# Kernel tuning notes

Measured on AMD Instinct MI355X. Metric: run time of the kernel, lower is better.

The kernel has to match this reference:

```python
import jax, jax.numpy as jnp
import numpy as np

CHEB_K = 2; HORIZON = 12; HFS = 4; D_HEAD = 32; EPS = 1e-5

def layer_norm(x, g, b):
    mu = x.mean(-1, keepdims=True)
    v = ((x - mu) ** 2).mean(-1, keepdims=True)
    return (x - mu) * jax.lax.rsqrt(v + EPS) * g + b

def gconv(x, supports, W, b):
    # x:[B,N,C], supports:[K,N,N], W:[N,K,C,O], b:[N,O]
    xg = jnp.einsum('knm,bmc->bnkc', supports, x)
    return jnp.einsum('bnkc,nkco->bno', xg, W) + b

def run_layer(x, state0, supports, gW, gb, uW, ub):
    # x:[B,T,N,C] -> hidden states [B,T,N,H] via GRU-style adaptive graph-conv recurrence
    def step(state, xt):
        xs = jnp.concatenate([xt, state], -1)
        zr = jax.nn.sigmoid(gconv(xs, supports, gW, gb))
        z, r = jnp.split(zr, 2, -1)
        hc = jnp.tanh(gconv(jnp.concatenate([xt, z * state], -1), supports, uW, ub))
        h = r * state + (1.0 - r) * hc
        return h, h
    _, hs = jax.lax.scan(step, state0, x.transpose(1, 0, 2, 3))
    return hs.transpose(1, 0, 2, 3)

def setup_inputs():
    key = jax.random.key(0)
    B, T, N, Din, H, E = 32, 12, 512, 2, 64, 16
    ks = iter(jax.random.split(key, 40))
    def rn(shape, scale):
        return jax.random.normal(next(ks), shape, jnp.float32) * scale
    inp = {}
    inp['source'] = rn((B, T, N, Din), 1.0)
    inp['targets'] = rn((B, T, N, 1), 1.0)
    inp['node_emb'] = rn((N, E), 1.0)
    for l, din in enumerate([Din, H]):
        c = din + H
        inp['gate_wpool_%d' % l] = rn((E, CHEB_K, c, 2 * H), (E * CHEB_K * c) ** -0.5)
        inp['gate_bpool_%d' % l] = rn((E, 2 * H), E ** -0.5)
        inp['upd_wpool_%d' % l] = rn((E, CHEB_K, c, H), (E * CHEB_K * c) ** -0.5)
        inp['upd_bpool_%d' % l] = rn((E, H), E ** -0.5)
    hyp_in = CHEB_K * H * CHEB_K * H
    inp['hyp_W'] = rn((hyp_in, HORIZON * HFS), hyp_in ** -0.5)
    inp['hyp_b'] = rn((HORIZON * HFS,), 0.02)
    for nm in ['Wq', 'Wk', 'Wv', 'ffW1', 'ffW2']:
        inp[nm] = rn((H, H), H ** -0.5)
    for nm in ['bq', 'bk', 'bv', 'ffb1', 'ffb2']:
        inp[nm] = jnp.zeros((H,), jnp.float32)
    inp['ln1_g'] = jnp.ones((H,), jnp.float32); inp['ln1_b'] = jnp.zeros((H,), jnp.float32)
    inp['ln2_g'] = jnp.ones((H,), jnp.float32); inp['ln2_b'] = jnp.zeros((H,), jnp.float32)
    inp['fc_W'] = rn((H, 1), H ** -0.5)
    inp['fc_b'] = jnp.zeros((1,), jnp.float32)
    return inp

def reference(source, targets, node_emb, gate_wpool_0, gate_bpool_0, upd_wpool_0, upd_bpool_0,
              gate_wpool_1, gate_bpool_1, upd_wpool_1, upd_bpool_1, hyp_W, hyp_b,
              Wq, bq, Wk, bk, Wv, bv, ln1_g, ln1_b, ffW1, ffb1, ffW2, ffb2, ln2_g, ln2_b, fc_W, fc_b):
    B, T, N, _ = source.shape
    H = Wq.shape[0]
    # adaptive supports (cheb_k = 2): [I, softmax(relu(E @ E^T), dim=1)]
    adj = jax.nn.softmax(jax.nn.relu(node_emb @ node_emb.T), axis=1)
    supports = jnp.stack([jnp.eye(N, dtype=source.dtype), adj], 0)  # [K,N,N]
    state0 = jnp.zeros((B, N, H), source.dtype)
    out = source
    for (gwp, gbp, uwp, ubp) in [(gate_wpool_0, gate_bpool_0, upd_wpool_0, upd_bpool_0),
                                 (gate_wpool_1, gate_bpool_1, upd_wpool_1, upd_bpool_1)]:
        gW = jnp.einsum('ne,ekio->nkio', node_emb, gwp); gb = node_emb @ gbp
        uW = jnp.einsum('ne,ekio->nkio', node_emb, uwp); ub = node_emb @ ubp
        out = run_layer(out, state0, supports, gW, gb, uW, ub)
        last_uW = uW  # encoder returns last layer's candidate-gconv per-node weights
    # Hypernetwork: dilation=0 grouped 1xHFS conv == scale last hidden state by sum of filter taps
    hlin = last_uW.reshape(N, -1) @ hyp_W + hyp_b               # [N, horizon*HFS]
    fs = hlin.reshape(N, HORIZON, HFS).sum(-1)                  # [N, horizon]
    h = jnp.einsum('bnh,nt->btnh', out[:, -1], fs)              # [B, horizon, N, H]
    # Transform attention block (L = 1; loop re-uses same `out`, only last iter matters)
    heads = H // D_HEAD
    q = out @ Wq + bq; k = out @ Wk + bk; v = h @ Wv + bv
    def split_heads(t):
        return t.reshape(B, T, N, heads, D_HEAD).transpose(3, 0, 2, 1, 4)  # [h,B,N,T,d]
    q, k, v = split_heads(q), split_heads(k), split_heads(v)
    A = jax.nn.softmax(jnp.einsum('hbntd,hbnsd->hbnts', q, k) / (D_HEAD ** 0.5), axis=-1)
    o = jnp.einsum('hbnts,hbnsd->hbntd', A, v)
    o = o.transpose(1, 3, 2, 0, 4).reshape(B, T, N, H)
    val = layer_norm(o + out, ln1_g, ln1_b)
    ffo = jnp.maximum(val @ ffW1 + ffb1, 0.0) @ ffW2 + ffb2
    out_h = layer_norm(ffo + val, ln2_g, ln2_b)
    y = (out_h @ fc_W + fc_b)[..., 0]                           # [B,T,N]
    y = y.reshape(-1, HORIZON, 1, N).transpose(0, 1, 3, 2)      # [B,horizon,N,1]
    return y
```

## Files before the change

### kernel.cpp

```cpp
#include <hip/hip_runtime.h>
#include <hip/hip_bf16.h>


using bf16 = __hip_bfloat16;
#define B2F(x) __bfloat162float(x)

#define NN 512
#define BBATCH 32
#define HHID 64
#define TT 12
#define EE 16

typedef __attribute__((ext_vector_type(4))) float f32x4;
typedef __attribute__((ext_vector_type(8))) short bf16x8;

__device__ inline float wsum(float x) {
#pragma unroll
  for (int off = 32; off > 0; off >>= 1) x += __shfl_xor(x, off, 64);
  return x;
}

__device__ inline uint4 llc_load4(const void* p) {
  uint4 r;
  asm volatile("global_load_dwordx4 %0, %1, off sc0 sc1" : "=v"(r) : "v"(p));
  return r;
}
__device__ inline uint2 llc_load2(const void* p) {
  uint2 r;
  asm volatile("global_load_dwordx2 %0, %1, off sc0 sc1" : "=v"(r) : "v"(p));
  return r;
}
__device__ inline unsigned llc_load1(const void* p) {
  unsigned r;
  asm volatile("global_load_dword %0, %1, off sc0 sc1" : "=v"(r) : "v"(p));
  return r;
}
__device__ inline void llc_store_bf(void* p, unsigned short v) {
  asm volatile("global_store_short %0, %1, off sc0 sc1" :: "v"(p), "v"((unsigned)v) : "memory");
}
__device__ inline void llc_store_u1(void* p, unsigned v) {
  asm volatile("global_store_dword %0, %1, off sc0 sc1" :: "v"(p), "v"(v) : "memory");
}
template <int N> __device__ inline void wait_vmcnt() {
  if constexpr (N == 0) asm volatile("s_waitcnt vmcnt(0)" ::: "memory");
  else if constexpr (N == 1) asm volatile("s_waitcnt vmcnt(1)" ::: "memory");
  else if constexpr (N == 2) asm volatile("s_waitcnt vmcnt(2)" ::: "memory");
  else asm volatile("s_waitcnt vmcnt(4)" ::: "memory");
}

__device__ inline void lds_barrier() {
  asm volatile("s_waitcnt lgkmcnt(0)" ::: "memory");
  __builtin_amdgcn_s_barrier();
  asm volatile("" ::: "memory");
}

__device__ inline void gbar(unsigned* __restrict__ bar, int& cnt) {
  cnt++;
  __syncthreads();
  unsigned tgt = (unsigned)cnt;
  unsigned* flags = bar + 32;
  if (blockIdx.x == 0) {
    if (threadIdx.x < 64) {
      if (threadIdx.x == 0) llc_store_u1(flags, tgt);
      const unsigned* fp = flags + threadIdx.x * 8;
      bool ok;
      do {
        unsigned v0 = llc_load1(fp + 0), v1 = llc_load1(fp + 1),
                 v2 = llc_load1(fp + 2), v3 = llc_load1(fp + 3),
                 v4 = llc_load1(fp + 4), v5 = llc_load1(fp + 5),
                 v6 = llc_load1(fp + 6), v7 = llc_load1(fp + 7);
        wait_vmcnt<0>();
        __builtin_amdgcn_sched_barrier(0);
        ok = ((int)(v0 - tgt) >= 0) && ((int)(v1 - tgt) >= 0) &&
             ((int)(v2 - tgt) >= 0) && ((int)(v3 - tgt) >= 0) &&
             ((int)(v4 - tgt) >= 0) && ((int)(v5 - tgt) >= 0) &&
             ((int)(v6 - tgt) >= 0) && ((int)(v7 - tgt) >= 0);
      } while (!__all(ok));
      if (threadIdx.x == 0) llc_store_u1(bar, tgt);
    }
  } else if (threadIdx.x == 0) {
    llc_store_u1(flags + blockIdx.x, tgt);
    for (;;) {
      unsigned e = llc_load1(bar);
      wait_vmcnt<0>();
      __builtin_amdgcn_sched_barrier(0);
      if ((int)(e - tgt) >= 0) break;
      __builtin_amdgcn_s_sleep(2);
    }
  }
  __syncthreads();
}

__global__ __launch_bounds__(256) void zero_f32_kernel(float* __restrict__ p, int n) {
  int i = blockIdx.x * 256 + threadIdx.x;
  if (i < n) p[i] = 0.0f;
}


__global__ __launch_bounds__(256) void adj_kernel(const float* __restrict__ emb,
                                                  bf16* __restrict__ adjb) {
  __shared__ float embAll[NN * EE];
  __shared__ float red[256];
  int tid = threadIdx.x, n = blockIdx.x;
  for (int i = tid; i < NN * EE; i += 256) embAll[i] = emb[i];
  __syncthreads();
  float v[2];
#pragma unroll
  for (int j = 0; j < 2; j++) {
    int m = tid + j * 256;
    float s = 0.f;
#pragma unroll
    for (int e = 0; e < EE; e++) s += embAll[n * EE + e] * embAll[m * EE + e];
    v[j] = fmaxf(s, 0.0f);
  }
  float mx = fmaxf(v[0], v[1]);
  red[tid] = mx; __syncthreads();
  for (int s = 128; s > 0; s >>= 1) { if (tid < s) red[tid] = fmaxf(red[tid], red[tid + s]); __syncthreads(); }
  mx = red[0]; __syncthreads();
  float e0 = expf(v[0] - mx), e1 = expf(v[1] - mx);
  red[tid] = e0 + e1; __syncthreads();
  for (int s = 128; s > 0; s >>= 1) { if (tid < s) red[tid] += red[tid + s]; __syncthreads(); }
  float inv = 1.0f / red[0];
  adjb[n * NN + tid] = __float2bfloat16(e0 * inv);
  adjb[n * NN + tid + 256] = __float2bfloat16(e1 * inv);
}

__global__ __launch_bounds__(256) void wgen_kernel(const float* __restrict__ pool,
                                                   const float* __restrict__ emb,
                                                   float* __restrict__ out, int J) {
  __shared__ float embL[128 * EE];
  int tid = threadIdx.x;
  int n0 = blockIdx.y * 128;
  for (int i = tid; i < 128 * EE; i += 256) embL[i] = emb[n0 * EE + i];
  __syncthreads();
  int j = blockIdx.x * 256 + tid;
  if (j >= J) return;
  float pw[EE];
#pragma unroll
  for (int e = 0; e < EE; e++) pw[e] = pool[e * J + j];
#pragma unroll 4
  for (int nn = 0; nn < 128; nn++) {
    float s = 0.f;
#pragma unroll
    for (int e = 0; e < EE; e++) s += embL[nn * EE + e] * pw[e];
    out[(size_t)(n0 + nn) * J + j] = s;
  }
}

__global__ __launch_bounds__(256) void wgen_t_kernel(const float* __restrict__ pool,
                                                     const float* __restrict__ emb,
                                                     bf16* __restrict__ out, int J,
                                                     int O, int KCP, int KC) {
  __shared__ float embL[128 * EE];
  int tid = threadIdx.x;
  int n0 = blockIdx.y * 128;
  for (int i = tid; i < 128 * EE; i += 256) embL[i] = emb[n0 * EE + i];
  __syncthreads();
  int p = blockIdx.x * 256 + tid;
  unsigned kc = (unsigned)p % (unsigned)KCP;
  unsigned o = (unsigned)p / (unsigned)KCP;
  size_t P = (size_t)KCP * O;
  if (kc >= (unsigned)KC) {
    bf16 z = __float2bfloat16(0.f);
    for (int nn = 0; nn < 128; nn++) out[(size_t)(n0 + nn) * P + p] = z;
    return;
  }
  int jp = (int)kc * O + (int)o;
  float pw[EE];
#pragma unroll
  for (int e = 0; e < EE; e++) pw[e] = pool[e * J + jp];
#pragma unroll 4
  for (int nn = 0; nn < 128; nn++) {
    float s = 0.f;
#pragma unroll
    for (int e = 0; e < EE; e++) s += embL[nn * EE + e] * pw[e];
    out[(size_t)(n0 + nn) * P + p] = __float2bfloat16(s);
  }
}

__global__ __launch_bounds__(256) void pw_kernel(const float* __restrict__ upool,
                                                 const float* __restrict__ hypW,
                                                 float* __restrict__ PW) {
  __shared__ float red[256];
  int j = blockIdx.x, e = blockIdx.y, tid = threadIdx.x;
  float s = 0.f;
#pragma unroll 4
  for (int p = tid; p < 16384; p += 256) s += upool[e * 16384 + p] * hypW[p * 48 + j];
  red[tid] = s; __syncthreads();
  for (int t = 128; t > 0; t >>= 1) { if (tid < t) red[tid] += red[tid + t]; __syncthreads(); }
  if (tid == 0) PW[e * 48 + j] = red[0];
}

__global__ __launch_bounds__(256) void fs_kernel(const float* __restrict__ emb,
                                                 const float* __restrict__ PW,
                                                 const float* __restrict__ hypb,
                                                 float* __restrict__ fs) {
  int id = blockIdx.x * 256 + threadIdx.x;
  if (id >= NN * TT) return;
  int n = id / TT, t = id % TT;
  float s = 0.f;
#pragma unroll
  for (int f = 0; f < 4; f++) {
    int j = t * 4 + f;
    float h = hypb[j];
#pragma unroll
    for (int e = 0; e < EE; e++) h += emb[n * EE + e] * PW[e * 48 + j];
    s += h;
  }
  fs[id] = s;
}

__global__ __launch_bounds__(256) void cvt_src_kernel(const float* __restrict__ src,
                                                      bf16* __restrict__ x) {
  int id = blockIdx.x * 256 + threadIdx.x;
  int c = id & 1, b = (id >> 1) & 31, n = (id >> 6) & 511, t = id >> 15;
  x[id] = __float2bfloat16(src[((b * TT + t) * NN + n) * 2 + c]);
}

#define DBUF 4672

__device__ inline void xsT_wr8(unsigned short* xsT, int base, int q0l, int k, uint4 v) {
  union { uint4 u; unsigned short h[8]; } cv; cv.u = v;
#pragma unroll
  for (int qq = 0; qq < 8; qq++) {
    int q = q0l + qq;
    xsT[base + q * 72 + (q >> 3) * 8 + k] = cv.h[qq];
  }
}

template <int QW>
__device__ inline void diffuse_tileP(const bf16x8* __restrict__ apre,
                                     const bf16* __restrict__ X, bf16* __restrict__ Y,
                                     int Q, int n0, int q0, char* smraw, int tid) {
  constexpr int LPC = QW / 32;
  constexpr int NCT = QW / 16;
  unsigned short* xsT = (unsigned short*)smraw;
  int w = tid >> 6, lane = tid & 63;
  int col = lane & 15, quad = lane >> 4;
  int kr, ql;
  if constexpr (QW == 64) { kr = tid >> 3; ql = (tid & 7) * 8; }
  else                    { kr = tid >> 2; ql = (tid & 3) * 8; }
  f32x4 acc[NCT];
#pragma unroll
  for (int ct = 0; ct < NCT; ct++) acc[ct] = (f32x4){0.f, 0.f, 0.f, 0.f};
  const bf16* Xb = X + q0 + ql;
  uint4 pre[3][LPC];
#pragma unroll
  for (int d = 0; d < 3; d++) {
    pre[d][0] = llc_load4(Xb + (size_t)(d * 64 + kr) * Q);
    if constexpr (QW == 64)
      pre[d][1] = llc_load4(Xb + (size_t)(d * 64 + 32 + kr) * Q);
  }
  wait_vmcnt<2 * LPC>();
  xsT_wr8(xsT, 0, ql, kr, pre[0][0]);
  if constexpr (QW == 64) xsT_wr8(xsT, 0, ql, 32 + kr, pre[0][1]);
  pre[0][0] = llc_load4(Xb + (size_t)(3 * 64 + kr) * Q);
  if constexpr (QW == 64)
    pre[0][1] = llc_load4(Xb + (size_t)(3 * 64 + 32 + kr) * Q);
  lds_barrier();
#pragma unroll
  for (int c = 0; c < 8; c++) {
    int sl = (c + 1) % 3;
    if (c < 7) {
      if (c < 5) wait_vmcnt<2 * LPC>();
      else if (c == 5) wait_vmcnt<LPC>();
      else wait_vmcnt<0>();
      int nb = ((c + 1) & 1) * DBUF;
      xsT_wr8(xsT, nb, ql, kr, pre[sl][0]);
      if constexpr (QW == 64) xsT_wr8(xsT, nb, ql, 32 + kr, pre[sl][1]);
    }
    int base = (c & 1) * DBUF;
#pragma unroll
    for (int ki = 0; ki < 2; ki++) {
      bf16x8 a = apre[c * 2 + ki];
#pragma unroll
      for (int ct = 0; ct < NCT; ct++) {
        int q = ct * 16 + col;
        bf16x8 b = *(const bf16x8*)&xsT[base + q * 72 + (q >> 3) * 8 + ki * 32 + quad * 8];
        acc[ct] = __builtin_amdgcn_mfma_f32_16x16x32_bf16(a, b, acc[ct], 0, 0, 0);
      }
    }
    if (c + 4 < 8) {
      pre[sl][0] = llc_load4(Xb + (size_t)((c + 4) * 64 + kr) * Q);
      if constexpr (QW == 64)
        pre[sl][1] = llc_load4(Xb + (size_t)((c + 4) * 64 + 32 + kr) * Q);
    }
    lds_barrier();
  }
#pragma unroll
  for (int ct = 0; ct < NCT; ct++)
#pragma unroll
    for (int r = 0; r < 4; r++) {
      int row = n0 + w * 16 + quad * 4 + r;
      bf16 hb = __float2bfloat16(acc[ct][r]);
      llc_store_bf(Y + (size_t)row * Q + q0 + ct * 16 + col, *(unsigned short*)&hb);
    }
}


template <int C>
__device__ inline void stage_A(int n, int tid, unsigned short* xinb,
    const bf16* __restrict__ xt, const bf16* __restrict__ xd,
    const bf16* __restrict__ sa, const bf16* __restrict__ sad) {
  constexpr int cc = C + HHID, KC = 2 * cc, KCP = (KC + 31) & ~31, PIT = KCP + 8;
  __syncthreads();
  for (int i = tid; i < 32 * KCP; i += 256) {
    int b = i / KCP, kc = i - b * KCP;
    unsigned short v = 0;
    if (kc < C)            v = *(const unsigned short*)&xt[(n * 32 + b) * C + kc];
    else if (kc < cc)      v = *(const unsigned short*)&sa[(n * 32 + b) * HHID + kc - C];
    else if (kc < cc + C)  v = *(const unsigned short*)&xd[(n * 32 + b) * C + kc - cc];
    else if (kc < KC)      v = *(const unsigned short*)&sad[(n * 32 + b) * HHID + kc - cc - C];
    xinb[b * PIT + kc] = v;
  }
  __syncthreads();
}

template <int C>
__device__ inline void gate_epilogue(int n, int w, int col, int quad,
    f32x4 acc[2][2], const float* __restrict__ gb, const float* __restrict__ state,
    bf16* __restrict__ zs, bf16* __restrict__ rbuf) {
#pragma unroll
  for (int i = 0; i < 2; i++) {
    int o = (w + i * 4) * 16 + col;
    float bv = gb[n * 128 + o];
#pragma unroll
    for (int mt = 0; mt < 2; mt++)
#pragma unroll
      for (int r = 0; r < 4; r++) {
        int m = mt * 16 + quad * 4 + r;
        float zr = 1.0f / (1.0f + expf(-(acc[i][mt][r] + bv)));
        int idx = (n * 32 + m) * HHID + (o & 63);
        if (o < HHID) zs[idx] = __float2bfloat16(zr * state[idx]);
        else          rbuf[idx] = __float2bfloat16(zr);
      }
  }
}

template <int C>
__device__ inline void upd_epilogue(int n, int w, int col, int quad,
    f32x4 acc[2], const float* __restrict__ ub, float* __restrict__ state,
    bf16* __restrict__ sb, const bf16* __restrict__ rbuf, bf16* __restrict__ xo) {
  int o = w * 16 + col;
  float bv = ub[n * 64 + o];
#pragma unroll
  for (int mt = 0; mt < 2; mt++)
#pragma unroll
    for (int r = 0; r < 4; r++) {
      int m = mt * 16 + quad * 4 + r;
      int idx = (n * 32 + m) * HHID + o;
      float hc = tanhf(acc[mt][r] + bv);
      float rr = B2F(rbuf[idx]);
      float st = state[idx];
      float h = rr * st + (1.0f - rr) * hc;
      state[idx] = h;
      bf16 hb = __float2bfloat16(h);
      sb[idx] = hb;
      xo[idx] = hb;
    }
}

template <int C>
__device__ inline void gate_mfma(int n, int tid, const unsigned short* xinb,
    const bf16* __restrict__ gWt, const float* __restrict__ gb,
    const float* __restrict__ state, bf16* __restrict__ zs, bf16* __restrict__ rbuf) {
  constexpr int KC = 2 * (C + HHID), KCP = (KC + 31) & ~31, PIT = KCP + 8;
  int w = tid >> 6, lane = tid & 63, col = lane & 15, quad = lane >> 4;
  f32x4 acc[2][2];
#pragma unroll
  for (int i = 0; i < 2; i++)
#pragma unroll
    for (int mt = 0; mt < 2; mt++) acc[i][mt] = (f32x4){0.f, 0.f, 0.f, 0.f};
  const bf16* Wn = gWt + (size_t)n * KCP * 128;
#pragma unroll 2
  for (int k0 = 0; k0 < KCP; k0 += 32) {
    int ko = k0 + quad * 8;
    bf16x8 a0 = *(const bf16x8*)&xinb[col * PIT + ko];
    bf16x8 a1 = *(const bf16x8*)&xinb[(16 + col) * PIT + ko];
#pragma unroll
    for (int i = 0; i < 2; i++) {
      int o = (w + i * 4) * 16 + col;
      bf16x8 bf = *(const bf16x8*)(Wn + (size_t)o * KCP + ko);
      acc[i][0] = __builtin_amdgcn_mfma_f32_16x16x32_bf16(a0, bf, acc[i][0], 0, 0, 0);
      acc[i][1] = __builtin_amdgcn_mfma_f32_16x16x32_bf16(a1, bf, acc[i][1], 0, 0, 0);
    }
  }
  gate_epilogue<C>(n, w, col, quad, acc, gb, state, zs, rbuf);
}

template <int C>
__device__ inline void upd_mfma(int n, int tid, const unsigned short* xinb,
    const bf16* __restrict__ uWt, const float* __restrict__ ub,
    float* __restrict__ state, bf16* __restrict__ sb,
    const bf16* __restrict__ rbuf, bf16* __restrict__ xo) {
  constexpr int KC = 2 * (C + HHID), KCP = (KC + 31) & ~31, PIT = KCP + 8;
  int w = tid >> 6, lane = tid & 63, col = lane & 15, quad = lane >> 4;
  f32x4 acc[2];
  acc[0] = (f32x4){0.f, 0.f, 0.f, 0.f};
  acc[1] = (f32x4){0.f, 0.f, 0.f, 0.f};
  const bf16* Wn = uWt + (size_t)n * KCP * 64;
  int o = w * 16 + col;
#pragma unroll 2
  for (int k0 = 0; k0 < KCP; k0 += 32) {
    int ko = k0 + quad * 8;
    bf16x8 a0 = *(const bf16x8*)&xinb[col * PIT + ko];
    bf16x8 a1 = *(const bf16x8*)&xinb[(16 + col) * PIT + ko];
    bf16x8 bf = *(const bf16x8*)(Wn + (size_t)o * KCP + ko);
    acc[0] = __builtin_amdgcn_mfma_f32_16x16x32_bf16(a0, bf, acc[0], 0, 0, 0);
    acc[1] = __builtin_amdgcn_mfma_f32_16x16x32_bf16(a1, bf, acc[1], 0, 0, 0);
  }
  upd_epilogue<C>(n, w, col, quad, acc, ub, state, sb, rbuf, xo);
}


template <int C>
__global__ __launch_bounds__(256, 2) void recur_kernel(
    const bf16* __restrict__ adjb, const bf16* __restrict__ xin,
    const bf16* __restrict__ gWt, const float* __restrict__ gb,
    const bf16* __restrict__ uWt, const float* __restrict__ ub,
    bf16* __restrict__ zs, bf16* __restrict__ sdiff, bf16* __restrict__ zsdiff,
    bf16* __restrict__ xd, bf16* __restrict__ xout, unsigned* __restrict__ bar) {
  constexpr int KC = 2 * (C + HHID), KCP = (KC + 31) & ~31, PIT = KCP + 8;
  constexpr int NK = KCP / 32;
  constexpr int QX = 32 * C;
  __shared__ __align__(16) char dsm[2 * DBUF * 2];
  __shared__ __align__(16) unsigned short xinb[32 * PIT];
  int bid = blockIdx.x, tid = threadIdx.x;
  int w = tid >> 6, lane = tid & 63, col = lane & 15, quad = lane >> 4;
  int bcnt = 0;

  bf16x8 apre[16];
  {
    int n0p = ((bid & 255) >> 5) * 64;
    const bf16* ar = adjb + (size_t)(n0p + w * 16 + col) * NN;
#pragma unroll
    for (int c = 0; c < 8; c++)
#pragma unroll
      for (int ki = 0; ki < 2; ki++)
        apre[c * 2 + ki] = *(const bf16x8*)(ar + c * 64 + ki * 32 + quad * 8);
  }
  bf16x8 fg[2 * NK];
  {
    const bf16* Wn = gWt + (size_t)bid * KCP * 128;
#pragma unroll
    for (int i = 0; i < 2; i++) {
      int o = (w + i * 4) * 16 + col;
#pragma unroll
      for (int kk = 0; kk < NK; kk++)
        fg[i * NK + kk] = *(const bf16x8*)(Wn + (size_t)o * KCP + kk * 32 + quad * 8);
    }
  }
  bf16x8 fu[NK];
  {
    const bf16* Wn = uWt + (size_t)bid * KCP * 64;
    int o = w * 16 + col;
#pragma unroll
    for (int kk = 0; kk < NK; kk++)
      fu[kk] = *(const bf16x8*)(Wn + (size_t)o * KCP + kk * 32 + quad * 8);
  }
  float gbv0 = gb[bid * 128 + w * 16 + col];
  float gbv1 = gb[bid * 128 + 64 + w * 16 + col];
  float ubv  = ub[bid * 64 + w * 16 + col];

  for (int i = tid; i < 32 * PIT; i += 256) xinb[i] = 0;
  __syncthreads();

  int r2 = tid >> 3, ch = tid & 7;
  uint4 vxt; unsigned sxt = 0, sxd = 0;
  if constexpr (C == 64) {
    vxt = *(const uint4*)(xin + (size_t)(bid * 32 + r2) * 64 + ch * 8);
  } else {
    if (tid < 32) sxt = *(const unsigned*)(xin + (size_t)(bid * 32 + tid) * 2);
  }

  float st[2][4], rr_[2][4];
#pragma unroll
  for (int mt = 0; mt < 2; mt++)
#pragma unroll
    for (int r4 = 0; r4 < 4; r4++) st[mt][r4] = 0.f;

  if constexpr (C == 2) {
    int wg = (bid & 31) | ((bid >> 8) << 5);
    if (wg < TT)
      diffuse_tileP<64>(apre, xin + (size_t)wg * NN * QX, xd + (size_t)wg * NN * QX,
                        QX, ((bid & 255) >> 5) * 64, 0, dsm, tid);
  } else {
    if (bid >= 256)
      diffuse_tileP<64>(apre, xin, xd, 2048, ((bid & 255) >> 5) * 64,
                        (bid & 31) * 64, dsm, tid);
  }
  gbar(bar, bcnt);

  for (int t = 0; t < TT; t++) {
    const bf16* xt = xin + (size_t)t * NN * QX;
    const bf16* xdt = (C == 2) ? (xd + (size_t)t * NN * QX) : xd;
    bf16* xo = xout + (size_t)t * NN * 32 * HHID;
    if (t > 0) {
      const bf16* sbp = xout + (size_t)(t - 1) * NN * 32 * HHID;
      if constexpr (C == 64) {
        if (bid < 256)
          diffuse_tileP<64>(apre, sbp, sdiff, 2048, (bid >> 5) * 64,
                            (bid & 31) * 64, dsm, tid);
        else
          diffuse_tileP<64>(apre, xt, xd, 2048, ((bid & 255) >> 5) * 64,
                            (bid & 31) * 64, dsm, tid);
      } else {
        int cs = (bid & 31) | ((bid >> 8) << 5);
        diffuse_tileP<32>(apre, sbp, sdiff, 2048, ((bid & 255) >> 5) * 64,
                          cs * 32, dsm, tid);
      }
      gbar(bar, bcnt);
    }
    if constexpr (C == 64) {
      *(uint4*)&xinb[r2 * PIT + ch * 8] = vxt;
      uint4 v1 = llc_load4(xdt + (size_t)(bid * 32 + r2) * 64 + ch * 8);
      uint4 v2;
      if (t > 0) v2 = llc_load4(sdiff + (size_t)(bid * 32 + r2) * 64 + ch * 8);
      wait_vmcnt<0>();
      *(uint4*)&xinb[r2 * PIT + 128 + ch * 8] = v1;
      if (t > 0) *(uint4*)&xinb[r2 * PIT + 192 + ch * 8] = v2;
    } else {
      if (tid < 32) *(unsigned*)&xinb[tid * PIT] = sxt;
      if (t == 0) {
        if (tid < 32) {
          unsigned v = llc_load1(xdt + (size_t)(bid * 32 + tid) * 2);
          wait_vmcnt<0>();
          *(unsigned*)&xinb[tid * PIT + 66] = v;
        }
      } else {
        if (tid >= 32 && tid < 64) *(unsigned*)&xinb[(tid - 32) * PIT + 66] = sxd;
        int r2a = tid >> 4, c4 = tid & 15;
        uint2 va = llc_load2(sdiff + (size_t)(bid * 32 + r2a) * 64 + c4 * 4);
        uint2 vb = llc_load2(sdiff + (size_t)(bid * 32 + 16 + r2a) * 64 + c4 * 4);
        wait_vmcnt<0>();
        *(uint2*)&xinb[r2a * PIT + 68 + c4 * 4] = va;
        *(uint2*)&xinb[(16 + r2a) * PIT + 68 + c4 * 4] = vb;
      }
    }
    __syncthreads();
    {
      f32x4 acc[2][2];
#pragma unroll
      for (int i = 0; i < 2; i++)
#pragma unroll
        for (int mt = 0; mt < 2; mt++) acc[i][mt] = (f32x4){0.f, 0.f, 0.f, 0.f};
#pragma unroll
      for (int kk = 0; kk < NK; kk++) {
        int ko = kk * 32 + quad * 8;
        bf16x8 a0 = *(const bf16x8*)&xinb[col * PIT + ko];
        bf16x8 a1 = *(const bf16x8*)&xinb[(16 + col) * PIT + ko];
#pragma unroll
        for (int i = 0; i < 2; i++) {
          acc[i][0] = __builtin_amdgcn_mfma_f32_16x16x32_bf16(a0, fg[i * NK + kk], acc[i][0], 0, 0, 0);
          acc[i][1] = __builtin_amdgcn_mfma_f32_16x16x32_bf16(a1, fg[i * NK + kk], acc[i][1], 0, 0, 0);
        }
      }
      __syncthreads();
#pragma unroll
      for (int mt = 0; mt < 2; mt++)
#pragma unroll
        for (int r4 = 0; r4 < 4; r4++) {
          int m = mt * 16 + quad * 4 + r4;
          float z = 1.0f / (1.0f + expf(-(acc[0][mt][r4] + gbv0)));
          float rv = 1.0f / (1.0f + expf(-(acc[1][mt][r4] + gbv1)));
          rr_[mt][r4] = rv;
          bf16 zb = __float2bfloat16(z * st[mt][r4]);
          xinb[m * PIT + C + w * 16 + col] = *(unsigned short*)&zb;
          llc_store_bf(zs + (size_t)(bid * 32 + m) * 64 + w * 16 + col,
                       *(unsigned short*)&zb);
        }
    }
    if (t > 0) {
      gbar(bar, bcnt);
      {
        int cs = (bid & 31) | ((bid >> 8) << 5);
        diffuse_tileP<32>(apre, zs, zsdiff, 2048, ((bid & 255) >> 5) * 64,
                          cs * 32, dsm, tid);
      }
      gbar(bar, bcnt);
      if constexpr (C == 64) {
        uint4 v = llc_load4(zsdiff + (size_t)(bid * 32 + r2) * 64 + ch * 8);
        wait_vmcnt<0>();
        *(uint4*)&xinb[r2 * PIT + 192 + ch * 8] = v;
      } else {
        int r2a = tid >> 4, c4 = tid & 15;
        uint2 va = llc_load2(zsdiff + (size_t)(bid * 32 + r2a) * 64 + c4 * 4);
        uint2 vb = llc_load2(zsdiff + (size_t)(bid * 32 + 16 + r2a) * 64 + c4 * 4);
        wait_vmcnt<0>();
        *(uint2*)&xinb[r2a * PIT + 68 + c4 * 4] = va;
        *(uint2*)&xinb[(16 + r2a) * PIT + 68 + c4 * 4] = vb;
      }
    }
    __syncthreads();
    {
      f32x4 acc[2];
      acc[0] = (f32x4){0.f, 0.f, 0.f, 0.f};
      acc[1] = (f32x4){0.f, 0.f, 0.f, 0.f};
#pragma unroll
      for (int kk = 0; kk < NK; kk++) {
        int ko = kk * 32 + quad * 8;
        bf16x8 a0 = *(const bf16x8*)&xinb[col * PIT + ko];
        bf16x8 a1 = *(const bf16x8*)&xinb[(16 + col) * PIT + ko];
        acc[0] = __builtin_amdgcn_mfma_f32_16x16x32_bf16(a0, fu[kk], acc[0], 0, 0, 0);
        acc[1] = __builtin_amdgcn_mfma_f32_16x16x32_bf16(a1, fu[kk], acc[1], 0, 0, 0);
      }
      __syncthreads();
      if (t + 1 < TT) {
        if constexpr (C == 64) {
          vxt = *(const uint4*)(xin + (size_t)(t + 1) * NN * QX +
                                (size_t)(bid * 32 + r2) * 64 + ch * 8);
        } else {
          if (tid < 32)
            sxt = *(const unsigned*)(xin + (size_t)(t + 1) * NN * QX +
                                     (size_t)(bid * 32 + tid) * 2);
          else if (tid < 64)
            sxd = *(const unsigned*)(xd + (size_t)(t + 1) * NN * QX +
                                     (size_t)(bid * 32 + (tid - 32)) * 2);
        }
      }
#pragma unroll
      for (int mt = 0; mt < 2; mt++)
#pragma unroll
        for (int r4 = 0; r4 < 4; r4++) {
          int m = mt * 16 + quad * 4 + r4;
          float hc = tanhf(acc[mt][r4] + ubv);
          float rv = rr_[mt][r4];
          float h = rv * st[mt][r4] + (1.0f - rv) * hc;
          st[mt][r4] = h;
          bf16 hb = __float2bfloat16(h);
          xinb[m * PIT + C + w * 16 + col] = *(unsigned short*)&hb;
          llc_store_bf(xo + (size_t)(bid * 32 + m) * 64 + w * 16 + col,
                       *(unsigned short*)&hb);
        }
    }
    gbar(bar, bcnt);
  }
}


__global__ __launch_bounds__(256, 2) void diffuse0_kernel(const bf16* __restrict__ adjb,
                                                          const bf16* __restrict__ X,
                                                          bf16* __restrict__ Y) {
  __shared__ __align__(16) char smraw[2 * DBUF * 2];
  int bid = blockIdx.x, tid = threadIdx.x;
  int t = bid >> 3, n0 = (bid & 7) * 64;
  int w = tid >> 6, lane = tid & 63, col = lane & 15, quad = lane >> 4;
  bf16x8 ap[16];
  const bf16* ar = adjb + (size_t)(n0 + w * 16 + col) * NN;
#pragma unroll
  for (int c = 0; c < 8; c++)
#pragma unroll
    for (int ki = 0; ki < 2; ki++)
      ap[c * 2 + ki] = *(const bf16x8*)(ar + c * 64 + ki * 32 + quad * 8);
  diffuse_tileP<64>(ap, X + (size_t)t * NN * 64, Y + (size_t)t * NN * 64,
                    64, n0, 0, smraw, tid);
}

__global__ __launch_bounds__(256, 2) void diffuse1_kernel(const bf16* __restrict__ adjb,
                                                          const bf16* __restrict__ X,
                                                          bf16* __restrict__ Y) {
  __shared__ __align__(16) char smraw[2 * DBUF * 2];
  int bid = blockIdx.x, tid = threadIdx.x;
  int n0 = (bid >> 5) * 64;
  int w = tid >> 6, lane = tid & 63, col = lane & 15, quad = lane >> 4;
  bf16x8 ap[16];
  const bf16* ar = adjb + (size_t)(n0 + w * 16 + col) * NN;
#pragma unroll
  for (int c = 0; c < 8; c++)
#pragma unroll
    for (int ki = 0; ki < 2; ki++)
      ap[c * 2 + ki] = *(const bf16x8*)(ar + c * 64 + ki * 32 + quad * 8);
  diffuse_tileP<64>(ap, X, Y, 2048, n0, (bid & 31) * 64, smraw, tid);
}

template <int C>
__global__ __launch_bounds__(256, 2) void gate_wrap(
    const bf16* xt, const bf16* xdt, const bf16* sa, const bf16* sad,
    const bf16* gWt, const float* gb, const float* state, bf16* zs, bf16* rbuf) {
  constexpr int KC = 2 * (C + HHID), KCP = (KC + 31) & ~31, PIT = KCP + 8;
  __shared__ __align__(16) unsigned short xinb[32 * PIT];
  stage_A<C>(blockIdx.x, threadIdx.x, xinb, xt, xdt, sa, sad);
  gate_mfma<C>(blockIdx.x, threadIdx.x, xinb, gWt, gb, state, zs, rbuf);
}

template <int C>
__global__ __launch_bounds__(256, 2) void upd_wrap(
    const bf16* xt, const bf16* xdt, const bf16* sa, const bf16* sad,
    const bf16* uWt, const float* ub, float* state, bf16* sb,
    const bf16* rbuf, bf16* xo) {
  constexpr int KC = 2 * (C + HHID), KCP = (KC + 31) & ~31, PIT = KCP + 8;
  __shared__ __align__(16) unsigned short xinb[32 * PIT];
  stage_A<C>(blockIdx.x, threadIdx.x, xinb, xt, xdt, sa, sad);
  upd_mfma<C>(blockIdx.x, threadIdx.x, xinb, uWt, ub, state, sb, rbuf, xo);
}


#define TP 68

__global__ __launch_bounds__(256, 4) void attn1_kernel(
    const bf16* __restrict__ x1, const float* __restrict__ fsb,
    const float* __restrict__ Wq, const float* __restrict__ bq,
    const float* __restrict__ Wk, const float* __restrict__ bk,
    const float* __restrict__ Wv, const float* __restrict__ bv,
    const float* __restrict__ ln1g, const float* __restrict__ ln1b,
    bf16* __restrict__ val) {
  __shared__ bf16 WqT[4096], WkT[4096];
  __shared__ bf16 Wv_s[4096];
  __shared__ bf16 Xb[16 * 72];
  __shared__ float qs[TT * TP], ks[TT * TP];
  __shared__ float A[2 * TT * TT];
  __shared__ float ovv[64], fss[TT];
  __shared__ float bqs[64], bks[64], bvs[64], g1s[64], b1s[64];
  int tid = threadIdx.x;
  int w = tid >> 6, lane = tid & 63, col = lane & 15, quad = lane >> 4;
#pragma unroll
  for (int i = 0; i < 16; i++) {
    int e = tid * 16 + i;
    int hi = e >> 6, ho = e & 63;
    WqT[ho * 64 + hi] = __float2bfloat16(Wq[e]);
    WkT[ho * 64 + hi] = __float2bfloat16(Wk[e]);
  }
  for (int i = tid; i < 4096; i += 256) Wv_s[i] = __float2bfloat16(Wv[i]);
  for (int i = tid; i < 16 * 72; i += 256) Xb[i] = __float2bfloat16(0.f);
  if (tid < 64) {
    bqs[tid] = bq[tid]; bks[tid] = bk[tid]; bvs[tid] = bv[tid];
    g1s[tid] = ln1g[tid]; b1s[tid] = ln1b[tid];
  }
  __syncthreads();
  for (int g = 0; g < 8; g++) {
    int p = blockIdx.x * 8 + g;
    int b = p >> 9, n = p & 511;
    for (int i = tid; i < TT * 64; i += 256) {
      int t = i >> 6, j = i & 63;
      Xb[t * 72 + j] = x1[(((size_t)t * NN + n) * BBATCH + b) * HHID + j];
    }
    if (tid < TT) fss[tid] = fsb[n * TT + tid];
    __syncthreads();
    {
      f32x4 aq = (f32x4){0.f, 0.f, 0.f, 0.f};
      f32x4 ak = (f32x4){0.f, 0.f, 0.f, 0.f};
#pragma unroll
      for (int ki = 0; ki < 2; ki++) {
        bf16x8 af = *(const bf16x8*)&Xb[col * 72 + ki * 32 + quad * 8];
        bf16x8 bqf = *(const bf16x8*)&WqT[(w * 16 + col) * 64 + ki * 32 + quad * 8];
        bf16x8 bkf = *(const bf16x8*)&WkT[(w * 16 + col) * 64 + ki * 32 + quad * 8];
        aq = __builtin_amdgcn_mfma_f32_16x16x32_bf16(af, bqf, aq, 0, 0, 0);
        ak = __builtin_amdgcn_mfma_f32_16x16x32_bf16(af, bkf, ak, 0, 0, 0);
      }
#pragma unroll
      for (int r = 0; r < 4; r++) {
        int t = quad * 4 + r;
        if (t < TT) {
          int h = w * 16 + col;
          qs[t * TP + h] = aq[r] + bqs[h];
          ks[t * TP + h] = ak[r] + bks[h];
        }
      }
    }
    if (tid < 64) {
      float s = 0.f;
#pragma unroll 8
      for (int j = 0; j < 64; j++)
        s += B2F(Xb[11 * 72 + j]) * B2F(Wv_s[j * 64 + tid]);
      ovv[tid] = s;
    }
    __syncthreads();
    for (int i = tid; i < 2 * TT * TT; i += 256) {
      int hd = i / (TT * TT), ts = i % (TT * TT), t = ts / TT, s = ts % TT;
      float acc = 0.f;
#pragma unroll
      for (int d = 0; d < 32; d++) acc += qs[t * TP + hd * 32 + d] * ks[s * TP + hd * 32 + d];
      A[i] = acc * 0.17677669529663687f;
    }
    __syncthreads();
    if (tid < 2 * TT) {
      int hd = tid / TT, t = tid % TT;
      float* row = &A[hd * TT * TT + t * TT];
      float m = row[0];
      for (int s = 1; s < TT; s++) m = fmaxf(m, row[s]);
      float sm = 0.f;
      for (int s = 0; s < TT; s++) { float e = expf(row[s] - m); row[s] = e; sm += e; }
      float inv = 1.0f / sm;
      for (int s = 0; s < TT; s++) row[s] *= inv;
    }
    __syncthreads();
#pragma unroll
    for (int it = 0; it < 3; it++) {
      int i = it * 256 + tid;
      int t = i >> 6, h = i & 63, hd = h >> 5;
      float afs = 0.f;
#pragma unroll
      for (int s = 0; s < TT; s++) afs += A[hd * TT * TT + t * TT + s] * fss[s];
      float o = ovv[h] * afs + bvs[h];
      float x = o + B2F(Xb[t * 72 + h]);
      float mu = wsum(x) * (1.0f / 64.0f);
      float d = x - mu;
      float var = wsum(d * d) * (1.0f / 64.0f);
      float v = d * rsqrtf(var + 1e-5f) * g1s[h] + b1s[h];
      val[((size_t)(b * TT + t) * NN + n) * HHID + h] = __float2bfloat16(v);
    }
    __syncthreads();
  }
}

__global__ __launch_bounds__(256, 4) void ffn_kernel(
    const bf16* __restrict__ val, const float* __restrict__ W1, const float* __restrict__ b1,
    const float* __restrict__ W2, const float* __restrict__ b2,
    const float* __restrict__ ln2g, const float* __restrict__ ln2b,
    const float* __restrict__ fcW, const float* __restrict__ fcb,
    float* __restrict__ out, int rows_per_block) {
  __shared__ bf16 W1T[4096], W2T[4096];
  __shared__ bf16 Ab[16 * 72];
  __shared__ bf16 Hh[16 * 72], Hl[16 * 72];
  __shared__ float fout[16 * 68];
  __shared__ float b1s[64], b2s[64], g2s[64], bb2[64], fcs[64];
  int tid = threadIdx.x;
  int w = tid >> 6, lane = tid & 63, col = lane & 15, quad = lane >> 4;
#pragma unroll
  for (int i = 0; i < 16; i++) {
    int e = tid * 16 + i;
    int hi = e >> 6, ho = e & 63;
    W1T[ho * 64 + hi] = __float2bfloat16(W1[e]);
    W2T[ho * 64 + hi] = __float2bfloat16(W2[e]);
  }
  if (tid < 64) {
    b1s[tid] = b1[tid]; b2s[tid] = b2[tid];
    g2s[tid] = ln2g[tid]; bb2[tid] = ln2b[tid]; fcs[tid] = fcW[tid];
  }
  __syncthreads();
  float fcbv = fcb[0];
  for (int c0 = 0; c0 < rows_per_block; c0 += 16) {
    size_t r0 = (size_t)blockIdx.x * rows_per_block + c0;
    for (int i = tid; i < 1024; i += 256) {
      int rr = i >> 6, j = i & 63;
      Ab[rr * 72 + j] = val[(r0 + rr) * 64 + j];
    }
    __syncthreads();
    {
      f32x4 a1 = (f32x4){0.f, 0.f, 0.f, 0.f};
#pragma unroll
      for (int ki = 0; ki < 2; ki++) {
        bf16x8 af = *(const bf16x8*)&Ab[col * 72 + ki * 32 + quad * 8];
        bf16x8 bf1 = *(const bf16x8*)&W1T[(w * 16 + col) * 64 + ki * 32 + quad * 8];
        a1 = __builtin_amdgcn_mfma_f32_16x16x32_bf16(af, bf1, a1, 0, 0, 0);
      }
#pragma unroll
      for (int r = 0; r < 4; r++) {
        int m = quad * 4 + r, h = w * 16 + col;
        float hv = fmaxf(a1[r] + b1s[h], 0.0f);
        bf16 hb = __float2bfloat16(hv);
        float lo = hv - B2F(hb);
        Hh[m * 72 + h] = hb;
        Hl[m * 72 + h] = __float2bfloat16(lo);
      }
    }
    __syncthreads();
    {
      f32x4 a2 = (f32x4){0.f, 0.f, 0.f, 0.f};
#pragma unroll
      for (int ki = 0; ki < 2; ki++) {
        bf16x8 ah = *(const bf16x8*)&Hh[col * 72 + ki * 32 + quad * 8];
        bf16x8 al = *(const bf16x8*)&Hl[col * 72 + ki * 32 + quad * 8];
        bf16x8 bf2 = *(const bf16x8*)&W2T[(w * 16 + col) * 64 + ki * 32 + quad * 8];
        a2 = __builtin_amdgcn_mfma_f32_16x16x32_bf16(ah, bf2, a2, 0, 0, 0);
        a2 = __builtin_amdgcn_mfma_f32_16x16x32_bf16(al, bf2, a2, 0, 0, 0);
      }
#pragma unroll
      for (int r = 0; r < 4; r++) {
        int m = quad * 4 + r, h = w * 16 + col;
        fout[m * 68 + h] = a2[r] + b2s[h] + B2F(Ab[m * 72 + h]);
      }
    }
    __syncthreads();
#pragma unroll
    for (int p4 = 0; p4 < 4; p4++) {
      int m = p4 * 4 + w;
      float y = fout[m * 68 + lane];
      float mu = wsum(y) * (1.0f / 64.0f);
      float d = y - mu;
      float var = wsum(d * d) * (1.0f / 64.0f);
      float oh = d * rsqrtf(var + 1e-5f) * g2s[lane] + bb2[lane];
      float contrib = wsum(oh * fcs[lane]);
      if (lane == 0) out[r0 + m] = contrib + fcbv;
    }
    __syncthreads();
  }
}

extern "C" void kernel_launch(void* const* d_in, const int* in_sizes, int n_in,
                              void* d_out, int out_size, void* d_ws, size_t ws_size,
                              hipStream_t stream) {
  const float* src = (const float*)d_in[0];
  const float* emb = (const float*)d_in[2];
  const float* gwp[2] = {(const float*)d_in[3], (const float*)d_in[7]};
  const float* gbp[2] = {(const float*)d_in[4], (const float*)d_in[8]};
  const float* uwp[2] = {(const float*)d_in[5], (const float*)d_in[9]};
  const float* ubp[2] = {(const float*)d_in[6], (const float*)d_in[10]};
  const float* hypW = (const float*)d_in[11];
  const float* hypb = (const float*)d_in[12];
  const float *Wq, *Wk, *Wv, *ffW1, *ffW2, *bq, *bk, *bv, *ffb1, *ffb2;
  const float *ln1g, *ln1b, *ln2g, *ln2b, *fcW, *fcb;
  if (in_sizes[14] == 4096) {
    Wq = (const float*)d_in[13]; Wk = (const float*)d_in[14]; Wv = (const float*)d_in[15];
    ffW1 = (const float*)d_in[16]; ffW2 = (const float*)d_in[17];
    bq = (const float*)d_in[18]; bk = (const float*)d_in[19]; bv = (const float*)d_in[20];
    ffb1 = (const float*)d_in[21]; ffb2 = (const float*)d_in[22];
    ln1g = (const float*)d_in[23]; ln1b = (const float*)d_in[24];
    ln2g = (const float*)d_in[25]; ln2b = (const float*)d_in[26];
    fcW = (const float*)d_in[27]; fcb = (const float*)d_in[28];
  } else {
    Wq = (const float*)d_in[13]; bq = (const float*)d_in[14];
    Wk = (const float*)d_in[15]; bk = (const float*)d_in[16];
    Wv = (const float*)d_in[17]; bv = (const float*)d_in[18];
    ln1g = (const float*)d_in[19]; ln1b = (const float*)d_in[20];
    ffW1 = (const float*)d_in[21]; ffb1 = (const float*)d_in[22];
    ffW2 = (const float*)d_in[23]; ffb2 = (const float*)d_in[24];
    ln2g = (const float*)d_in[25]; ln2b = (const float*)d_in[26];
    fcW = (const float*)d_in[27]; fcb = (const float*)d_in[28];
  }
  float* outp = (float*)d_out;

  char* ws = (char*)d_ws;
  size_t off = 0;
  auto alloc = [&](size_t bytes) {
    void* p = ws + off;
    off += (bytes + 255) & ~(size_t)255;
    return p;
  };
  bf16* adjb = (bf16*)alloc((size_t)512 * 512 * 2);
  bf16* gWb = (bf16*)alloc((size_t)512 * 32768 * 2);
  bf16* uWb = (bf16*)alloc((size_t)512 * 16384 * 2);
  float* gb = (float*)alloc((size_t)512 * 128 * 4);
  float* ub = (float*)alloc((size_t)512 * 64 * 4);
  bf16* xin0 = (bf16*)alloc((size_t)12 * 512 * 32 * 2 * 2);
  bf16* x0 = (bf16*)alloc((size_t)12 * 512 * 32 * 64 * 2);
  bf16* xd0 = (bf16*)alloc((size_t)12 * 512 * 32 * 2 * 2);
  bf16* xdL1 = (bf16*)alloc((size_t)512 * 32 * 64 * 2);
  float* state = (float*)alloc((size_t)512 * 32 * 64 * 4);
  bf16* sb = (bf16*)alloc((size_t)512 * 32 * 64 * 2);
  bf16* sdiff = (bf16*)alloc((size_t)512 * 32 * 64 * 2);
  bf16* zs = (bf16*)alloc((size_t)512 * 32 * 64 * 2);
  bf16* zsdiff = (bf16*)alloc((size_t)512 * 32 * 64 * 2);
  bf16* rbuf = (bf16*)alloc((size_t)512 * 32 * 64 * 2);
  float* PW = (float*)alloc((size_t)16 * 48 * 4);
  float* fsb = (float*)alloc((size_t)512 * 12 * 4);
  unsigned* bar = (unsigned*)alloc((size_t)544 * 4);
  bf16* val = gWb;

  adj_kernel<<<512, 256, 0, stream>>>(emb, adjb);
  pw_kernel<<<dim3(48, 16), 256, 0, stream>>>(uwp[1], hypW, PW);
  fs_kernel<<<24, 256, 0, stream>>>(emb, PW, hypb, fsb);
  cvt_src_kernel<<<1536, 256, 0, stream>>>(src, xin0);

  int occ0 = 0, occ1 = 0;
  hipOccupancyMaxActiveBlocksPerMultiprocessor(&occ0, recur_kernel<2>, 256, 0);
  hipOccupancyMaxActiveBlocksPerMultiprocessor(&occ1, recur_kernel<64>, 256, 0);

  for (int l = 0; l < 2; l++) {
    int C = (l == 0) ? 2 : 64;
    int KC = 2 * (C + 64);
    int KCP = (KC + 31) & ~31;
    int JG = KC * 128, JU = KC * 64;
    wgen_t_kernel<<<dim3(KCP * 128 / 256, 4), 256, 0, stream>>>(
        gwp[l], emb, gWb, JG, 128, KCP, KC);
    wgen_t_kernel<<<dim3(KCP * 64 / 256, 4), 256, 0, stream>>>(
        uwp[l], emb, uWb, JU, 64, KCP, KC);
    wgen_kernel<<<dim3(1, 4), 256, 0, stream>>>(gbp[l], emb, gb, 128);
    wgen_kernel<<<dim3(1, 4), 256, 0, stream>>>(ubp[l], emb, ub, 64);
    zero_f32_kernel<<<3, 256, 0, stream>>>((float*)bar, 544);

    const bf16* xin = (l == 0) ? xin0 : x0;
    bf16* xd = (l == 0) ? xd0 : xdL1;
    int occ = (l == 0) ? occ0 : occ1;
    if (occ >= 2) {
      if (l == 0)
        recur_kernel<2><<<512, 256, 0, stream>>>(adjb, xin, gWb, gb, uWb, ub,
                                                 zs, sdiff, zsdiff, xd, x0, bar);
      else
        recur_kernel<64><<<512, 256, 0, stream>>>(adjb, xin, gWb, gb, uWb, ub,
                                                  zs, sdiff, zsdiff, xd, x0, bar);
    } else {
      zero_f32_kernel<<<4096, 256, 0, stream>>>(state, 512 * 32 * 64);
      zero_f32_kernel<<<2048, 256, 0, stream>>>((float*)sb, 512 * 32 * 64 / 2);
      if (l == 0) diffuse0_kernel<<<96, 256, 0, stream>>>(adjb, xin, xd);
      for (int t = 0; t < 12; t++) {
        const bf16* xt = xin + (size_t)t * 512 * 32 * C;
        const bf16* xdt = (l == 0) ? (xd + (size_t)t * 512 * 32 * C) : xd;
        bf16* xo = x0 + (size_t)t * 512 * 32 * 64;
        if (l == 1) diffuse1_kernel<<<256, 256, 0, stream>>>(adjb, xt, xd);
        diffuse1_kernel<<<256, 256, 0, stream>>>(adjb, sb, sdiff);
        if (l == 0)
          gate_wrap<2><<<512, 256, 0, stream>>>(xt, xdt, sb, sdiff, gWb, gb, state, zs, rbuf);
        else
          gate_wrap<64><<<512, 256, 0, stream>>>(xt, xdt, sb, sdiff, gWb, gb, state, zs, rbuf);
        diffuse1_kernel<<<256, 256, 0, stream>>>(adjb, zs, zsdiff);
        if (l == 0)
          upd_wrap<2><<<512, 256, 0, stream>>>(xt, xdt, zs, zsdiff, uWb, ub, state, sb, rbuf, xo);
        else
          upd_wrap<64><<<512, 256, 0, stream>>>(xt, xdt, zs, zsdiff, uWb, ub, state, sb, rbuf, xo);
      }
    }
  }

  attn1_kernel<<<2048, 256, 0, stream>>>(x0, fsb, Wq, bq, Wk, bk, Wv, bv, ln1g, ln1b, val);
  ffn_kernel<<<2048, 256, 0, stream>>>(val, ffW1, ffb1, ffW2, ffb2, ln2g, ln2b, fcW, fcb,
                                       outp, 96);
}
```

Baseline: 1.651 ms.

## Prefetch all diffusion chunks up front, transpose hypW, and pad weight LDS tiles

The diffusion tile now issues all eight chunk loads at once into an 8-slot register buffer and drains them with decreasing vmcnt waits, replacing the rolling 3-slot prefetch. This gives more memory-level parallelism inside the latency-bound recurrent step, at the cost of extra registers. A new transpose kernel makes the hypW reads in pw_kernel coalesced. The transposed weight tiles in the attention and FFN kernels are padded to a 72-element row stride to cut LDS bank conflicts.

```diff
diff --git a/kernel.cpp b/kernel.cpp
--- a/kernel.cpp
+++ b/kernel.cpp
@@ -42,10 +42,18 @@
   asm volatile("global_store_dword %0, %1, off sc0 sc1" :: "v"(p), "v"(v) : "memory");
 }
 template <int N> __device__ inline void wait_vmcnt() {
-  if constexpr (N == 0) asm volatile("s_waitcnt vmcnt(0)" ::: "memory");
+  if constexpr (N <= 0)      asm volatile("s_waitcnt vmcnt(0)" ::: "memory");
   else if constexpr (N == 1) asm volatile("s_waitcnt vmcnt(1)" ::: "memory");
   else if constexpr (N == 2) asm volatile("s_waitcnt vmcnt(2)" ::: "memory");
-  else asm volatile("s_waitcnt vmcnt(4)" ::: "memory");
+  else if constexpr (N == 3) asm volatile("s_waitcnt vmcnt(3)" ::: "memory");
+  else if constexpr (N == 4) asm volatile("s_waitcnt vmcnt(4)" ::: "memory");
+  else if constexpr (N == 5) asm volatile("s_waitcnt vmcnt(5)" ::: "memory");
+  else if constexpr (N == 6) asm volatile("s_waitcnt vmcnt(6)" ::: "memory");
+  else if constexpr (N == 7) asm volatile("s_waitcnt vmcnt(7)" ::: "memory");
+  else if constexpr (N == 8) asm volatile("s_waitcnt vmcnt(8)" ::: "memory");
+  else if constexpr (N == 10) asm volatile("s_waitcnt vmcnt(10)" ::: "memory");
+  else if constexpr (N == 12) asm volatile("s_waitcnt vmcnt(12)" ::: "memory");
+  else                       asm volatile("s_waitcnt vmcnt(14)" ::: "memory");
 }
 
 __device__ inline void lds_barrier() {
@@ -178,14 +186,30 @@
   }
 }
 
+__global__ __launch_bounds__(256) void hypwT_kernel(const float* __restrict__ hypW,
+                                                    float* __restrict__ hypWT) {
+  __shared__ float tile[48 * 33];
+  int r0 = blockIdx.x * 32, tid = threadIdx.x;
+  for (int i = tid; i < 32 * 48; i += 256) {
+    int r = i / 48, c = i - r * 48;
+    tile[c * 33 + r] = hypW[(size_t)(r0 + r) * 48 + c];
+  }
+  __syncthreads();
+  for (int i = tid; i < 48 * 32; i += 256) {
+    int c = i >> 5, r = i & 31;
+    hypWT[(size_t)c * 16384 + r0 + r] = tile[c * 33 + r];
+  }
+}
+
 __global__ __launch_bounds__(256) void pw_kernel(const float* __restrict__ upool,
-                                                 const float* __restrict__ hypW,
+                                                 const float* __restrict__ hypWT,
                                                  float* __restrict__ PW) {
   __shared__ float red[256];
   int j = blockIdx.x, e = blockIdx.y, tid = threadIdx.x;
   float s = 0.f;
 #pragma unroll 4
-  for (int p = tid; p < 16384; p += 256) s += upool[e * 16384 + p] * hypW[p * 48 + j];
+  for (int p = tid; p < 16384; p += 256)
+    s += upool[e * 16384 + p] * hypWT[(size_t)j * 16384 + p];
   red[tid] = s; __syncthreads();
   for (int t = 128; t > 0; t >>= 1) { if (tid < t) red[tid] += red[tid + t]; __syncthreads(); }
   if (tid == 0) PW[e * 48 + j] = red[0];
@@ -227,6 +251,30 @@
     xsT[base + q * 72 + (q >> 3) * 8 + k] = cv.h[qq];
   }
 }
+
+#define DIFF_STEP(cc)                                                         \
+  {                                                                           \
+    if constexpr ((cc) < 7) {                                                 \
+      wait_vmcnt<(6 - (cc)) * LPC>();                                         \
+      constexpr int nb = ((((cc) + 1) & 1)) * DBUF;                           \
+      xsT_wr8(xsT, nb, ql, kr, pre[((cc) + 1) & 7][0]);                       \
+      if constexpr (QW == 64)                                                 \
+        xsT_wr8(xsT, nb, ql, 32 + kr, pre[((cc) + 1) & 7][1]);                \
+    }                                                                         \
+    constexpr int base = ((cc) & 1) * DBUF;                                   \
+    _Pragma("unroll")                                                         \
+    for (int ki = 0; ki < 2; ki++) {                                          \
+      bf16x8 a = apre[(cc) * 2 + ki];                                         \
+      _Pragma("unroll")                                                       \
+      for (int ct = 0; ct < NCT; ct++) {                                      \
+        int q = ct * 16 + col;                                                \
+        bf16x8 b = *(const bf16x8*)&xsT[base + q * 72 + (q >> 3) * 8 +        \
+                                        ki * 32 + quad * 8];                  \
+        acc[ct] = __builtin_amdgcn_mfma_f32_16x16x32_bf16(a, b, acc[ct], 0, 0, 0); \
+      }                                                                       \
+    }                                                                         \
+    lds_barrier();                                                            \
+  }
 
 template <int QW>
 __device__ inline void diffuse_tileP(const bf16x8* __restrict__ apre,
@@ -244,49 +292,19 @@
 #pragma unroll
   for (int ct = 0; ct < NCT; ct++) acc[ct] = (f32x4){0.f, 0.f, 0.f, 0.f};
   const bf16* Xb = X + q0 + ql;
-  uint4 pre[3][LPC];
-#pragma unroll
-  for (int d = 0; d < 3; d++) {
-    pre[d][0] = llc_load4(Xb + (size_t)(d * 64 + kr) * Q);
+  uint4 pre[8][LPC];
+#pragma unroll
+  for (int c = 0; c < 8; c++) {
+    pre[c][0] = llc_load4(Xb + (size_t)(c * 64 + kr) * Q);
     if constexpr (QW == 64)
-      pre[d][1] = llc_load4(Xb + (size_t)(d * 64 + 32 + kr) * Q);
-  }
-  wait_vmcnt<2 * LPC>();
+      pre[c][1] = llc_load4(Xb + (size_t)(c * 64 + 32 + kr) * Q);
+  }
+  wait_vmcnt<7 * LPC>();
   xsT_wr8(xsT, 0, ql, kr, pre[0][0]);
   if constexpr (QW == 64) xsT_wr8(xsT, 0, ql, 32 + kr, pre[0][1]);
-  pre[0][0] = llc_load4(Xb + (size_t)(3 * 64 + kr) * Q);
-  if constexpr (QW == 64)
-    pre[0][1] = llc_load4(Xb + (size_t)(3 * 64 + 32 + kr) * Q);
   lds_barrier();
-#pragma unroll
-  for (int c = 0; c < 8; c++) {
-    int sl = (c + 1) % 3;
-    if (c < 7) {
-      if (c < 5) wait_vmcnt<2 * LPC>();
-      else if (c == 5) wait_vmcnt<LPC>();
-      else wait_vmcnt<0>();
-      int nb = ((c + 1) & 1) * DBUF;
-      xsT_wr8(xsT, nb, ql, kr, pre[sl][0]);
-      if constexpr (QW == 64) xsT_wr8(xsT, nb, ql, 32 + kr, pre[sl][1]);
-    }
-    int base = (c & 1) * DBUF;
-#pragma unroll
-    for (int ki = 0; ki < 2; ki++) {
-      bf16x8 a = apre[c * 2 + ki];
-#pragma unroll
-      for (int ct = 0; ct < NCT; ct++) {
-        int q = ct * 16 + col;
-        bf16x8 b = *(const bf16x8*)&xsT[base + q * 72 + (q >> 3) * 8 + ki * 32 + quad * 8];
-        acc[ct] = __builtin_amdgcn_mfma_f32_16x16x32_bf16(a, b, acc[ct], 0, 0, 0);
-      }
-    }
-    if (c + 4 < 8) {
-      pre[sl][0] = llc_load4(Xb + (size_t)((c + 4) * 64 + kr) * Q);
-      if constexpr (QW == 64)
-        pre[sl][1] = llc_load4(Xb + (size_t)((c + 4) * 64 + 32 + kr) * Q);
-    }
-    lds_barrier();
-  }
+  DIFF_STEP(0) DIFF_STEP(1) DIFF_STEP(2) DIFF_STEP(3)
+  DIFF_STEP(4) DIFF_STEP(5) DIFF_STEP(6) DIFF_STEP(7)
 #pragma unroll
   for (int ct = 0; ct < NCT; ct++)
 #pragma unroll
@@ -696,6 +714,7 @@
 
 
 #define TP 68
+#define WS 72
 
 __global__ __launch_bounds__(256, 4) void attn1_kernel(
     const bf16* __restrict__ x1, const float* __restrict__ fsb,
@@ -704,7 +723,7 @@
     const float* __restrict__ Wv, const float* __restrict__ bv,
     const float* __restrict__ ln1g, const float* __restrict__ ln1b,
     bf16* __restrict__ val) {
-  __shared__ bf16 WqT[4096], WkT[4096];
+  __shared__ bf16 WqT[WS * 64], WkT[WS * 64];
   __shared__ bf16 Wv_s[4096];
   __shared__ bf16 Xb[16 * 72];
   __shared__ float qs[TT * TP], ks[TT * TP];
@@ -717,8 +736,8 @@
   for (int i = 0; i < 16; i++) {
     int e = tid * 16 + i;
     int hi = e >> 6, ho = e & 63;
-    WqT[ho * 64 + hi] = __float2bfloat16(Wq[e]);
-    WkT[ho * 64 + hi] = __float2bfloat16(Wk[e]);
+    WqT[ho * WS + hi] = __float2bfloat16(Wq[e]);
+    WkT[ho * WS + hi] = __float2bfloat16(Wk[e]);
   }
   for (int i = tid; i < 4096; i += 256) Wv_s[i] = __float2bfloat16(Wv[i]);
   for (int i = tid; i < 16 * 72; i += 256) Xb[i] = __float2bfloat16(0.f);
@@ -742,8 +761,8 @@
 #pragma unroll
       for (int ki = 0; ki < 2; ki++) {
         bf16x8 af = *(const bf16x8*)&Xb[col * 72 + ki * 32 + quad * 8];
-        bf16x8 bqf = *(const bf16x8*)&WqT[(w * 16 + col) * 64 + ki * 32 + quad * 8];
-        bf16x8 bkf = *(const bf16x8*)&WkT[(w * 16 + col) * 64 + ki * 32 + quad * 8];
+        bf16x8 bqf = *(const bf16x8*)&WqT[(w * 16 + col) * WS + ki * 32 + quad * 8];
+        bf16x8 bkf = *(const bf16x8*)&WkT[(w * 16 + col) * WS + ki * 32 + quad * 8];
         aq = __builtin_amdgcn_mfma_f32_16x16x32_bf16(af, bqf, aq, 0, 0, 0);
         ak = __builtin_amdgcn_mfma_f32_16x16x32_bf16(af, bkf, ak, 0, 0, 0);
       }
@@ -809,7 +828,7 @@
     const float* __restrict__ ln2g, const float* __restrict__ ln2b,
     const float* __restrict__ fcW, const float* __restrict__ fcb,
     float* __restrict__ out, int rows_per_block) {
-  __shared__ bf16 W1T[4096], W2T[4096];
+  __shared__ bf16 W1T[WS * 64], W2T[WS * 64];
   __shared__ bf16 Ab[16 * 72];
   __shared__ bf16 Hh[16 * 72], Hl[16 * 72];
   __shared__ float fout[16 * 68];
@@ -820,8 +839,8 @@
   for (int i = 0; i < 16; i++) {
     int e = tid * 16 + i;
     int hi = e >> 6, ho = e & 63;
-    W1T[ho * 64 + hi] = __float2bfloat16(W1[e]);
-    W2T[ho * 64 + hi] = __float2bfloat16(W2[e]);
+    W1T[ho * WS + hi] = __float2bfloat16(W1[e]);
+    W2T[ho * WS + hi] = __float2bfloat16(W2[e]);
   }
   if (tid < 64) {
     b1s[tid] = b1[tid]; b2s[tid] = b2[tid];
@@ -841,7 +860,7 @@
 #pragma unroll
       for (int ki = 0; ki < 2; ki++) {
         bf16x8 af = *(const bf16x8*)&Ab[col * 72 + ki * 32 + quad * 8];
-        bf16x8 bf1 = *(const bf16x8*)&W1T[(w * 16 + col) * 64 + ki * 32 + quad * 8];
+        bf16x8 bf1 = *(const bf16x8*)&W1T[(w * 16 + col) * WS + ki * 32 + quad * 8];
         a1 = __builtin_amdgcn_mfma_f32_16x16x32_bf16(af, bf1, a1, 0, 0, 0);
       }
 #pragma unroll
@@ -861,7 +880,7 @@
       for (int ki = 0; ki < 2; ki++) {
         bf16x8 ah = *(const bf16x8*)&Hh[col * 72 + ki * 32 + quad * 8];
         bf16x8 al = *(const bf16x8*)&Hl[col * 72 + ki * 32 + quad * 8];
-        bf16x8 bf2 = *(const bf16x8*)&W2T[(w * 16 + col) * 64 + ki * 32 + quad * 8];
+        bf16x8 bf2 = *(const bf16x8*)&W2T[(w * 16 + col) * WS + ki * 32 + quad * 8];
         a2 = __builtin_amdgcn_mfma_f32_16x16x32_bf16(ah, bf2, a2, 0, 0, 0);
         a2 = __builtin_amdgcn_mfma_f32_16x16x32_bf16(al, bf2, a2, 0, 0, 0);
       }
@@ -945,10 +964,12 @@
   float* PW = (float*)alloc((size_t)16 * 48 * 4);
   float* fsb = (float*)alloc((size_t)512 * 12 * 4);
   unsigned* bar = (unsigned*)alloc((size_t)544 * 4);
+  float* hypWT = (float*)alloc((size_t)48 * 16384 * 4);
   bf16* val = gWb;
 
   adj_kernel<<<512, 256, 0, stream>>>(emb, adjb);
-  pw_kernel<<<dim3(48, 16), 256, 0, stream>>>(uwp[1], hypW, PW);
+  hypwT_kernel<<<512, 256, 0, stream>>>(hypW, hypWT);
+  pw_kernel<<<dim3(48, 16), 256, 0, stream>>>(uwp[1], hypWT, PW);
   fs_kernel<<<24, 256, 0, stream>>>(emb, PW, hypb, fsb);
   cvt_src_kernel<<<1536, 256, 0, stream>>>(src, xin0);
 
```

New measurement: 1.624 ms. About the same (-1.6%).
